# Optimization experiments

Hardware: AMD Instinct MI355X
Metric: run time of the kernel (lower is better)

## Reference

```python
import jax, jax.numpy as jnp
import numpy as np

N_NODES = 100000
N_EDGES = 1600000
IN_CH = 64
HID = 64
OUT_CH = 16
T = 1.0


def _gat_layer(x, edge_index, W, b, t):
    # x: [N, d_in]; W: [d_out, d_in] (torch Linear weight layout); b: [d_out]
    N = x.shape[0]
    loop = jnp.arange(N, dtype=edge_index.dtype)
    src = jnp.concatenate([edge_index[0], loop])  # add self loops
    dst = jnp.concatenate([edge_index[1], loop])
    h = x @ W.T  # [N, d_out]
    x_i = h[dst]  # target node features per edge
    x_j = h[src]  # source node features per edge
    alpha = jnp.sum(x_i * x_j, axis=-1)  # [E']
    alpha = jnp.where(alpha > 0, jnp.asarray(t, h.dtype), jnp.asarray(-t, h.dtype))
    # segment softmax grouped by edge_index[0] (source), faithful to original
    m = jax.ops.segment_max(alpha, src, num_segments=N)
    e = jnp.exp(alpha - m[src])
    s = jax.ops.segment_sum(e, src, num_segments=N)
    w = e / s[src]
    msg = x_j * w[:, None]
    out = jax.ops.segment_sum(msg, dst, num_segments=N)  # scatter-add to target
    return out + b


def setup_inputs() -> dict:
    key = jax.random.key(0)
    k1, k2, k3, k4 = jax.random.split(key, 4)
    x = jax.random.normal(k1, (N_NODES, IN_CH), dtype=jnp.float32)
    edge_index = jax.random.randint(k2, (2, N_EDGES), 0, N_NODES, dtype=jnp.int64)
    # xavier-uniform-ish linear weights, torch layout [out, in]
    lim1 = float(np.sqrt(6.0 / (IN_CH + HID)))
    W1 = jax.random.uniform(k3, (HID, IN_CH), jnp.float32, -lim1, lim1)
    lim2 = float(np.sqrt(6.0 / (HID + OUT_CH)))
    W2 = jax.random.uniform(k4, (OUT_CH, HID), jnp.float32, -lim2, lim2)
    b1 = jnp.zeros((HID,), jnp.float32)
    b2 = jnp.zeros((OUT_CH,), jnp.float32)
    return {"x": x, "edge_index": edge_index, "W1": W1, "b1": b1, "W2": W2, "b2": b2}


def reference(x, edge_index, W1, b1, W2, b2):
    h = _gat_layer(x, edge_index, W1, b1, T)
    h = jax.nn.relu(h)
    h = _gat_layer(h, edge_index, W2, b2, T)
    return jax.nn.log_softmax(h, axis=1)
```

## Files before the change

### kernel.cpp

```cpp
#include <hip/hip_runtime.h>

#define EXPC 0.13533528323661270f
#define REP 8
#define CHUNK 16384

__global__ void zero_i32(int* __restrict__ p, int n) {
  int i = blockIdx.x * blockDim.x + threadIdx.x;
  if (i < n) p[i] = 0;
}

template <bool RELU_IN>
__global__ void __launch_bounds__(256, 1)
gemm64_k(const float* __restrict__ x, const float* __restrict__ W,
         float* __restrict__ h, int N) {
  __shared__ float xs[64][68];
  __shared__ float wt[64][68];
  const int t = threadIdx.x;
  const int r0 = blockIdx.x * 64;
  for (int i = t; i < 4096; i += 256) {
    int c = i >> 6, k = i & 63;
    wt[k][c] = W[i];
  }
  for (int s = t; s < 1024; s += 256) {
    int r = s >> 4, c4 = (s & 15) << 2;
    float4 v = make_float4(0.f, 0.f, 0.f, 0.f);
    if (r0 + r < N) {
      v = *(const float4*)(x + (size_t)(r0 + r) * 64 + c4);
      if (RELU_IN) {
        v.x = fmaxf(v.x, 0.f); v.y = fmaxf(v.y, 0.f);
        v.z = fmaxf(v.z, 0.f); v.w = fmaxf(v.w, 0.f);
      }
    }
    *(float4*)(&xs[r][c4]) = v;
  }
  __syncthreads();
  const int ty = t >> 4, tx = t & 15;
  float acc[4][4] = {};
  for (int kk = 0; kk < 64; kk += 4) {
    float4 a[4], w[4];
#pragma unroll
    for (int i = 0; i < 4; i++) a[i] = *(const float4*)(&xs[4 * ty + i][kk]);
#pragma unroll
    for (int m = 0; m < 4; m++) w[m] = *(const float4*)(&wt[kk + m][4 * tx]);
#pragma unroll
    for (int i = 0; i < 4; i++) {
      acc[i][0] = fmaf(a[i].x, w[0].x, fmaf(a[i].y, w[1].x,
                  fmaf(a[i].z, w[2].x, fmaf(a[i].w, w[3].x, acc[i][0]))));
      acc[i][1] = fmaf(a[i].x, w[0].y, fmaf(a[i].y, w[1].y,
                  fmaf(a[i].z, w[2].y, fmaf(a[i].w, w[3].y, acc[i][1]))));
      acc[i][2] = fmaf(a[i].x, w[0].z, fmaf(a[i].y, w[1].z,
                  fmaf(a[i].z, w[2].z, fmaf(a[i].w, w[3].z, acc[i][2]))));
      acc[i][3] = fmaf(a[i].x, w[0].w, fmaf(a[i].y, w[1].w,
                  fmaf(a[i].z, w[2].w, fmaf(a[i].w, w[3].w, acc[i][3]))));
    }
  }
#pragma unroll
  for (int i = 0; i < 4; i++) {
    int row = r0 + 4 * ty + i;
    if (row < N)
      *(float4*)(h + (size_t)row * 64 + 4 * tx) =
          make_float4(acc[i][0], acc[i][1], acc[i][2], acc[i][3]);
  }
}

template <bool RELU_IN>
__global__ void __launch_bounds__(256, 2)
gemm16_k(const float* __restrict__ x, const float* __restrict__ W,
         float* __restrict__ h, int N) {
  __shared__ float xs[64][68];
  __shared__ float wt[64][20];
  const int t = threadIdx.x;
  const int r0 = blockIdx.x * 64;
  for (int i = t; i < 1024; i += 256) {
    int c = i >> 6, k = i & 63;
    wt[k][c] = W[i];
  }
  for (int s = t; s < 1024; s += 256) {
    int r = s >> 4, c4 = (s & 15) << 2;
    float4 v = make_float4(0.f, 0.f, 0.f, 0.f);
    if (r0 + r < N) {
      v = *(const float4*)(x + (size_t)(r0 + r) * 64 + c4);
      if (RELU_IN) {
        v.x = fmaxf(v.x, 0.f); v.y = fmaxf(v.y, 0.f);
        v.z = fmaxf(v.z, 0.f); v.w = fmaxf(v.w, 0.f);
      }
    }
    *(float4*)(&xs[r][c4]) = v;
  }
  __syncthreads();
  const int r = t >> 2, j = (t & 3) << 2;
  float4 acc = make_float4(0.f, 0.f, 0.f, 0.f);
  for (int k = 0; k < 64; k++) {
    float a = xs[r][k];
    float4 w = *(const float4*)(&wt[k][j]);
    acc.x = fmaf(a, w.x, acc.x);
    acc.y = fmaf(a, w.y, acc.y);
    acc.z = fmaf(a, w.z, acc.z);
    acc.w = fmaf(a, w.w, acc.w);
  }
  int row = r0 + r;
  if (row < N) *(float4*)(h + (size_t)row * 16 + j) = acc;
}

__global__ void passA_k(const int* __restrict__ ei, int* __restrict__ chd,
                        int* __restrict__ chs, int E, int Et) {
  __shared__ int ld[512], ls[512];
  int t = threadIdx.x;
  for (int i = t; i < 512; i += 256) { ld[i] = 0; ls[i] = 0; }
  __syncthreads();
  int base = blockIdx.x * CHUNK;
  int end = base + CHUNK; if (end > Et) end = Et;
  for (int e = base + t; e < end; e += 256) {
    int s, d;
    if (e < E) { s = ei[e]; d = ei[E + e]; } else { s = e - E; d = s; }
    atomicAdd(&ld[d >> 8], 1);
    atomicAdd(&ls[s >> 8], 1);
  }
  __syncthreads();
  for (int i = t; i < 512; i += 256) {
    if (ld[i]) atomicAdd(chd + i, ld[i]);
    if (ls[i]) atomicAdd(chs + i, ls[i]);
  }
}

__global__ void scan2_k(const int* __restrict__ chd, const int* __restrict__ chs,
                        int* __restrict__ cbd, int* __restrict__ cbs,
                        int* __restrict__ cud, int* __restrict__ cus, int NB) {
  __shared__ int l[512];
  int t = threadIdx.x;
  for (int pass = 0; pass < 2; ++pass) {
    const int* src = pass ? chs : chd;
    int* db = pass ? cbs : cbd;
    int* dc = pass ? cus : cud;
    int v = (t < NB) ? src[t] : 0;
    l[t] = v;
    __syncthreads();
    for (int o = 1; o < 512; o <<= 1) {
      int a = (t >= o) ? l[t - o] : 0;
      __syncthreads();
      l[t] += a;
      __syncthreads();
    }
    if (t < NB) { int e = l[t] - v; db[t] = e; dc[t] = e; }
    __syncthreads();
  }
}

__global__ void passB_k(const int* __restrict__ ei, int* __restrict__ cud,
                        int* __restrict__ cus, int* __restrict__ part_dst,
                        unsigned char* __restrict__ part_src, int E, int Et) {
  __shared__ int cntd[512], cnts[512], based[512], bases[512];
  int t = threadIdx.x;
  for (int i = t; i < 512; i += 256) { cntd[i] = 0; cnts[i] = 0; }
  __syncthreads();
  int base = blockIdx.x * CHUNK;
  int end = base + CHUNK; if (end > Et) end = Et;
  for (int e = base + t; e < end; e += 256) {
    int s, d;
    if (e < E) { s = ei[e]; d = ei[E + e]; } else { s = e - E; d = s; }
    atomicAdd(&cntd[d >> 8], 1);
    atomicAdd(&cnts[s >> 8], 1);
  }
  __syncthreads();
  for (int i = t; i < 512; i += 256) {
    based[i] = cntd[i] ? atomicAdd(cud + i, cntd[i]) : 0;
    bases[i] = cnts[i] ? atomicAdd(cus + i, cnts[i]) : 0;
    cntd[i] = 0; cnts[i] = 0;
  }
  __syncthreads();
  for (int e = base + t; e < end; e += 256) {
    int s, d;
    if (e < E) { s = ei[e]; d = ei[E + e]; } else { s = e - E; d = s; }
    int bd = d >> 8, bs = s >> 8;
    int rd = atomicAdd(&cntd[bd], 1);
    int rs = atomicAdd(&cnts[bs], 1);
    part_dst[based[bd] + rd] = s | ((d & 255) << 17);
    part_src[bases[bs] + rs] = (unsigned char)(s & 255);
  }
}

__global__ void passC_k(const int* __restrict__ part_dst, const int* __restrict__ cbd,
                        const int* __restrict__ chd, int* __restrict__ csr_src,
                        int* __restrict__ in_deg, int* __restrict__ off, int N) {
  __shared__ int hist[256], loff[256], rank[256];
  int b = blockIdx.x, t = threadIdx.x;
  int segbase = cbd[b], segcnt = chd[b];
  hist[t] = 0; rank[t] = 0;
  __syncthreads();
  for (int i = t; i < segcnt; i += 256)
    atomicAdd(&hist[part_dst[segbase + i] >> 17], 1);
  __syncthreads();
  int x = hist[t];
  loff[t] = x;
  __syncthreads();
  for (int o = 1; o < 256; o <<= 1) {
    int a = (t >= o) ? loff[t - o] : 0;
    __syncthreads();
    loff[t] += a;
    __syncthreads();
  }
  int excl = loff[t] - x;
  int node = (b << 8) + t;
  if (node < N) { in_deg[node] = x; off[node] = segbase + excl; }
  __syncthreads();
  loff[t] = excl;
  __syncthreads();
  for (int i = t; i < segcnt; i += 256) {
    int rec = part_dst[segbase + i];
    int dl = rec >> 17;
    int r = atomicAdd(&rank[dl], 1);
    csr_src[segbase + loff[dl] + r] = rec & 0x1FFFF;
  }
}

__global__ void passCs_k(const unsigned char* __restrict__ part_src,
                         const int* __restrict__ cbs, const int* __restrict__ chs,
                         int* __restrict__ deg, int N) {
  __shared__ int hist[256];
  int b = blockIdx.x, t = threadIdx.x;
  int segbase = cbs[b], segcnt = chs[b];
  hist[t] = 0;
  __syncthreads();
  for (int i = t; i < segcnt; i += 256)
    atomicAdd(&hist[part_src[segbase + i]], 1);
  __syncthreads();
  int node = (b << 8) + t;
  if (node < N) deg[node] = hist[t];
}

template <int D>
__global__ void alpha_csr_k(const int* __restrict__ csr_src, const int* __restrict__ off,
                            const int* __restrict__ indeg, const float* __restrict__ h,
                            unsigned char* __restrict__ flagb, int* __restrict__ pos_rep,
                            int N) {
  const int G = D / 4;
  int t = blockIdx.x * 256 + threadIdx.x;
  int node = t / G;
  int c = t & (G - 1);
  if (node >= N) return;
  int* pos = pos_rep + (blockIdx.x & (REP - 1)) * N;
  const float4 hd = *(const float4*)(h + (size_t)node * D + c * 4);
  int j = off[node];
  int je = j + indeg[node];
  for (; j + 4 <= je; j += 4) {
    int s0 = csr_src[j], s1 = csr_src[j + 1], s2 = csr_src[j + 2], s3 = csr_src[j + 3];
    float4 a0 = *(const float4*)(h + (size_t)s0 * D + c * 4);
    float4 a1 = *(const float4*)(h + (size_t)s1 * D + c * 4);
    float4 a2 = *(const float4*)(h + (size_t)s2 * D + c * 4);
    float4 a3 = *(const float4*)(h + (size_t)s3 * D + c * 4);
    float p0 = fmaf(a0.x, hd.x, fmaf(a0.y, hd.y, fmaf(a0.z, hd.z, a0.w * hd.w)));
    float p1 = fmaf(a1.x, hd.x, fmaf(a1.y, hd.y, fmaf(a1.z, hd.z, a1.w * hd.w)));
    float p2 = fmaf(a2.x, hd.x, fmaf(a2.y, hd.y, fmaf(a2.z, hd.z, a2.w * hd.w)));
    float p3 = fmaf(a3.x, hd.x, fmaf(a3.y, hd.y, fmaf(a3.z, hd.z, a3.w * hd.w)));
#pragma unroll
    for (int o = G / 2; o > 0; o >>= 1) {
      p0 += __shfl_xor(p0, o);
      p1 += __shfl_xor(p1, o);
      p2 += __shfl_xor(p2, o);
      p3 += __shfl_xor(p3, o);
    }
    if (c == 0) {
      bool z0 = p0 > 0.f, z1 = p1 > 0.f, z2 = p2 > 0.f, z3 = p3 > 0.f;
      flagb[j] = z0; flagb[j + 1] = z1; flagb[j + 2] = z2; flagb[j + 3] = z3;
      if (z0) atomicAdd(pos + s0, 1);
      if (z1) atomicAdd(pos + s1, 1);
      if (z2) atomicAdd(pos + s2, 1);
      if (z3) atomicAdd(pos + s3, 1);
    }
  }
  for (; j < je; ++j) {
    int s = csr_src[j];
    float4 hs = *(const float4*)(h + (size_t)s * D + c * 4);
    float p = fmaf(hs.x, hd.x, fmaf(hs.y, hd.y, fmaf(hs.z, hd.z, hs.w * hd.w)));
#pragma unroll
    for (int o = G / 2; o > 0; o >>= 1) p += __shfl_xor(p, o);
    if (c == 0) {
      bool pz = p > 0.f;
      flagb[j] = (unsigned char)pz;
      if (pz) atomicAdd(pos + s, 1);
    }
  }
}

template <int D>
__global__ void denom_scale_k(const int* __restrict__ pos_rep, const int* __restrict__ deg,
                              float* __restrict__ h, int N) {
  const int G = D / 4;
  int t = blockIdx.x * 256 + threadIdx.x;
  int node = t / G;
  int c = t & (G - 1);
  if (node >= N) return;
  float dinv = 0.f;
  if (c == 0) {
    int p = 0;
#pragma unroll
    for (int r = 0; r < REP; r++) p += pos_rep[r * N + node];
    int dg = deg[node];
    dinv = (p > 0) ? 1.f / ((float)p + (float)(dg - p) * EXPC)
                   : 1.f / (EXPC * (float)dg);
  }
  dinv = __shfl(dinv, 0, G);
  float4* hp = (float4*)(h + (size_t)node * D + c * 4);
  float4 v = *hp;
  v.x *= dinv; v.y *= dinv; v.z *= dinv; v.w *= dinv;
  *hp = v;
}

template <int D, bool FUSE_LSM>
__global__ void gather_csr_k(const int* __restrict__ csr_src, const int* __restrict__ off,
                             const int* __restrict__ indeg,
                             const unsigned char* __restrict__ flagb,
                             const float* __restrict__ h,
                             const float* __restrict__ b, float* __restrict__ outp, int N) {
  const int G = D / 4;
  int t = blockIdx.x * 256 + threadIdx.x;
  int node = t / G;
  int c = t & (G - 1);
  if (node >= N) return;
  float4 acc = *(const float4*)(b + c * 4);
  int j = off[node];
  int je = j + indeg[node];
  for (; j + 4 <= je; j += 4) {
    int s0 = csr_src[j], s1 = csr_src[j + 1], s2 = csr_src[j + 2], s3 = csr_src[j + 3];
    float w0 = flagb[j] ? 1.f : EXPC;
    float w1 = flagb[j + 1] ? 1.f : EXPC;
    float w2 = flagb[j + 2] ? 1.f : EXPC;
    float w3 = flagb[j + 3] ? 1.f : EXPC;
    float4 v0 = *(const float4*)(h + (size_t)s0 * D + c * 4);
    float4 v1 = *(const float4*)(h + (size_t)s1 * D + c * 4);
    float4 v2 = *(const float4*)(h + (size_t)s2 * D + c * 4);
    float4 v3 = *(const float4*)(h + (size_t)s3 * D + c * 4);
    acc.x = fmaf(w0, v0.x, fmaf(w1, v1.x, fmaf(w2, v2.x, fmaf(w3, v3.x, acc.x))));
    acc.y = fmaf(w0, v0.y, fmaf(w1, v1.y, fmaf(w2, v2.y, fmaf(w3, v3.y, acc.y))));
    acc.z = fmaf(w0, v0.z, fmaf(w1, v1.z, fmaf(w2, v2.z, fmaf(w3, v3.z, acc.z))));
    acc.w = fmaf(w0, v0.w, fmaf(w1, v1.w, fmaf(w2, v2.w, fmaf(w3, v3.w, acc.w))));
  }
  for (; j < je; ++j) {
    int s = csr_src[j];
    float w = flagb[j] ? 1.f : EXPC;
    float4 hv = *(const float4*)(h + (size_t)s * D + c * 4);
    acc.x = fmaf(w, hv.x, acc.x);
    acc.y = fmaf(w, hv.y, acc.y);
    acc.z = fmaf(w, hv.z, acc.z);
    acc.w = fmaf(w, hv.w, acc.w);
  }
  if (FUSE_LSM) {
    float m = fmaxf(fmaxf(acc.x, acc.y), fmaxf(acc.z, acc.w));
    m = fmaxf(m, __shfl_xor(m, 1));
    m = fmaxf(m, __shfl_xor(m, 2));
    float s = expf(acc.x - m) + expf(acc.y - m) + expf(acc.z - m) + expf(acc.w - m);
    s += __shfl_xor(s, 1);
    s += __shfl_xor(s, 2);
    float lse = m + logf(s);
    acc.x -= lse; acc.y -= lse; acc.z -= lse; acc.w -= lse;
  }
  *(float4*)(outp + (size_t)node * D + c * 4) = acc;
}

extern "C" void kernel_launch(void* const* d_in, const int* in_sizes, int n_in,
                              void* d_out, int out_size, void* d_ws, size_t ws_size,
                              hipStream_t stream) {
  const float* x = (const float*)d_in[0];
  const int* ei = (const int*)d_in[1];
  const float* W1 = (const float*)d_in[2];
  const float* b1 = (const float*)d_in[3];
  const float* W2 = (const float*)d_in[4];
  const float* b2 = (const float*)d_in[5];
  float* out = (float*)d_out;

  const int N = in_sizes[0] / 64;
  const int E = in_sizes[1] / 2;
  const int Et = E + N;
  const int B = 256;
  const int nbT = (N + 63) / 64;
  const int NB = (N + 255) >> 8;
  const int nbP = (Et + CHUNK - 1) / CHUNK;

  char* ws = (char*)d_ws;
  float* h1 = (float*)ws;    ws += (size_t)N * 64 * 4;
  float* agg1 = (float*)ws;  ws += (size_t)N * 64 * 4;
  int* deg = (int*)ws;       ws += (size_t)N * 4;
  int* in_deg = (int*)ws;    ws += (size_t)N * 4;
  int* off = (int*)ws;       ws += (size_t)N * 4;
  int* chd = (int*)ws;       ws += 512 * 4;
  int* chs = (int*)ws;       ws += 512 * 4;
  int* cbd = (int*)ws;       ws += 512 * 4;
  int* cbs = (int*)ws;       ws += 512 * 4;
  int* cud = (int*)ws;       ws += 512 * 4;
  int* cus = (int*)ws;       ws += 512 * 4;
  int* csr_src = (int*)ws;   ws += (size_t)Et * 4;
  char* P = ws;              ws += (size_t)Et * 4 + (size_t)Et;
  int* part_dst = (int*)P;
  unsigned char* part_src = (unsigned char*)(P + (size_t)Et * 4);
  int* pos_rep = (int*)P;
  unsigned char* flagb = (unsigned char*)(P + (size_t)REP * N * 4);

  hipLaunchKernelGGL(zero_i32, dim3(4), dim3(B), 0, stream, chd, 1024);
  hipLaunchKernelGGL(passA_k, dim3(nbP), dim3(B), 0, stream, ei, chd, chs, E, Et);
  hipLaunchKernelGGL(scan2_k, dim3(1), dim3(512), 0, stream, chd, chs, cbd, cbs, cud, cus, NB);
  hipLaunchKernelGGL(passB_k, dim3(nbP), dim3(B), 0, stream, ei, cud, cus,
                     part_dst, part_src, E, Et);
  hipLaunchKernelGGL(passC_k, dim3(NB), dim3(B), 0, stream, part_dst, cbd, chd,
                     csr_src, in_deg, off, N);
  hipLaunchKernelGGL(passCs_k, dim3(NB), dim3(B), 0, stream, part_src, cbs, chs, deg, N);

  hipLaunchKernelGGL((gemm64_k<false>), dim3(nbT), dim3(B), 0, stream, x, W1, h1, N);
  hipLaunchKernelGGL(zero_i32, dim3((REP * N + B - 1) / B), dim3(B), 0, stream,
                     pos_rep, REP * N);
  hipLaunchKernelGGL((alpha_csr_k<64>), dim3(((size_t)N * 16 + B - 1) / B), dim3(B), 0,
                     stream, csr_src, off, in_deg, h1, flagb, pos_rep, N);
  hipLaunchKernelGGL((denom_scale_k<64>), dim3(((size_t)N * 16 + B - 1) / B), dim3(B), 0,
                     stream, pos_rep, deg, h1, N);
  hipLaunchKernelGGL((gather_csr_k<64, false>), dim3(((size_t)N * 16 + B - 1) / B), dim3(B),
                     0, stream, csr_src, off, in_deg, flagb, h1, b1, agg1, N);

  float* h2 = h1;
  hipLaunchKernelGGL((gemm16_k<true>), dim3(nbT), dim3(B), 0, stream, agg1, W2, h2, N);
  hipLaunchKernelGGL(zero_i32, dim3((REP * N + B - 1) / B), dim3(B), 0, stream,
                     pos_rep, REP * N);
  hipLaunchKernelGGL((alpha_csr_k<16>), dim3(((size_t)N * 4 + B - 1) / B), dim3(B), 0,
                     stream, csr_src, off, in_deg, h2, flagb, pos_rep, N);
  hipLaunchKernelGGL((denom_scale_k<16>), dim3(((size_t)N * 4 + B - 1) / B), dim3(B), 0,
                     stream, pos_rep, deg, h2, N);
  hipLaunchKernelGGL((gather_csr_k<16, true>), dim3(((size_t)N * 4 + B - 1) / B), dim3(B),
                     0, stream, csr_src, off, in_deg, flagb, h2, b2, out, N);
}
```

Before: 486.5 us.

## Fuse layer-2 GEMM and ReLU into layer-1 gather, unroll edge loops by 8

The layer-1 gather now applies ReLU and multiplies by W2 in registers: the 16 lanes of a node share the aggregated row through shuffles and write h2 directly. This removes the agg1 buffer write, the separate gemm16 kernel and its re-read of 64-wide rows. The alpha and gather edge loops are unrolled from 4 to 8 so more gathers are in flight at once, at the cost of more registers per thread. __launch_bounds__(256,1) is added to the alpha and gather kernels.

```diff
diff --git a/kernel.cpp b/kernel.cpp
--- a/kernel.cpp
+++ b/kernel.cpp
@@ -61,45 +61,6 @@
       *(float4*)(h + (size_t)row * 64 + 4 * tx) =
           make_float4(acc[i][0], acc[i][1], acc[i][2], acc[i][3]);
   }
-}
-
-template <bool RELU_IN>
-__global__ void __launch_bounds__(256, 2)
-gemm16_k(const float* __restrict__ x, const float* __restrict__ W,
-         float* __restrict__ h, int N) {
-  __shared__ float xs[64][68];
-  __shared__ float wt[64][20];
-  const int t = threadIdx.x;
-  const int r0 = blockIdx.x * 64;
-  for (int i = t; i < 1024; i += 256) {
-    int c = i >> 6, k = i & 63;
-    wt[k][c] = W[i];
-  }
-  for (int s = t; s < 1024; s += 256) {
-    int r = s >> 4, c4 = (s & 15) << 2;
-    float4 v = make_float4(0.f, 0.f, 0.f, 0.f);
-    if (r0 + r < N) {
-      v = *(const float4*)(x + (size_t)(r0 + r) * 64 + c4);
-      if (RELU_IN) {
-        v.x = fmaxf(v.x, 0.f); v.y = fmaxf(v.y, 0.f);
-        v.z = fmaxf(v.z, 0.f); v.w = fmaxf(v.w, 0.f);
-      }
-    }
-    *(float4*)(&xs[r][c4]) = v;
-  }
-  __syncthreads();
-  const int r = t >> 2, j = (t & 3) << 2;
-  float4 acc = make_float4(0.f, 0.f, 0.f, 0.f);
-  for (int k = 0; k < 64; k++) {
-    float a = xs[r][k];
-    float4 w = *(const float4*)(&wt[k][j]);
-    acc.x = fmaf(a, w.x, acc.x);
-    acc.y = fmaf(a, w.y, acc.y);
-    acc.z = fmaf(a, w.z, acc.z);
-    acc.w = fmaf(a, w.w, acc.w);
-  }
-  int row = r0 + r;
-  if (row < N) *(float4*)(h + (size_t)row * 16 + j) = acc;
 }
 
 __global__ void passA_k(const int* __restrict__ ei, int* __restrict__ chd,
@@ -229,10 +190,10 @@
 }
 
 template <int D>
-__global__ void alpha_csr_k(const int* __restrict__ csr_src, const int* __restrict__ off,
-                            const int* __restrict__ indeg, const float* __restrict__ h,
-                            unsigned char* __restrict__ flagb, int* __restrict__ pos_rep,
-                            int N) {
+__global__ void __launch_bounds__(256, 1)
+alpha_csr_k(const int* __restrict__ csr_src, const int* __restrict__ off,
+            const int* __restrict__ indeg, const float* __restrict__ h,
+            unsigned char* __restrict__ flagb, int* __restrict__ pos_rep, int N) {
   const int G = D / 4;
   int t = blockIdx.x * 256 + threadIdx.x;
   int node = t / G;
@@ -242,30 +203,29 @@
   const float4 hd = *(const float4*)(h + (size_t)node * D + c * 4);
   int j = off[node];
   int je = j + indeg[node];
-  for (; j + 4 <= je; j += 4) {
-    int s0 = csr_src[j], s1 = csr_src[j + 1], s2 = csr_src[j + 2], s3 = csr_src[j + 3];
-    float4 a0 = *(const float4*)(h + (size_t)s0 * D + c * 4);
-    float4 a1 = *(const float4*)(h + (size_t)s1 * D + c * 4);
-    float4 a2 = *(const float4*)(h + (size_t)s2 * D + c * 4);
-    float4 a3 = *(const float4*)(h + (size_t)s3 * D + c * 4);
-    float p0 = fmaf(a0.x, hd.x, fmaf(a0.y, hd.y, fmaf(a0.z, hd.z, a0.w * hd.w)));
-    float p1 = fmaf(a1.x, hd.x, fmaf(a1.y, hd.y, fmaf(a1.z, hd.z, a1.w * hd.w)));
-    float p2 = fmaf(a2.x, hd.x, fmaf(a2.y, hd.y, fmaf(a2.z, hd.z, a2.w * hd.w)));
-    float p3 = fmaf(a3.x, hd.x, fmaf(a3.y, hd.y, fmaf(a3.z, hd.z, a3.w * hd.w)));
+  for (; j + 8 <= je; j += 8) {
+    int s[8];
+    float4 a[8];
+#pragma unroll
+    for (int u = 0; u < 8; u++) s[u] = csr_src[j + u];
+#pragma unroll
+    for (int u = 0; u < 8; u++) a[u] = *(const float4*)(h + (size_t)s[u] * D + c * 4);
+    float p[8];
+#pragma unroll
+    for (int u = 0; u < 8; u++)
+      p[u] = fmaf(a[u].x, hd.x, fmaf(a[u].y, hd.y, fmaf(a[u].z, hd.z, a[u].w * hd.w)));
 #pragma unroll
     for (int o = G / 2; o > 0; o >>= 1) {
-      p0 += __shfl_xor(p0, o);
-      p1 += __shfl_xor(p1, o);
-      p2 += __shfl_xor(p2, o);
-      p3 += __shfl_xor(p3, o);
+#pragma unroll
+      for (int u = 0; u < 8; u++) p[u] += __shfl_xor(p[u], o);
     }
     if (c == 0) {
-      bool z0 = p0 > 0.f, z1 = p1 > 0.f, z2 = p2 > 0.f, z3 = p3 > 0.f;
-      flagb[j] = z0; flagb[j + 1] = z1; flagb[j + 2] = z2; flagb[j + 3] = z3;
-      if (z0) atomicAdd(pos + s0, 1);
-      if (z1) atomicAdd(pos + s1, 1);
-      if (z2) atomicAdd(pos + s2, 1);
-      if (z3) atomicAdd(pos + s3, 1);
+#pragma unroll
+      for (int u = 0; u < 8; u++) {
+        bool z = p[u] > 0.f;
+        flagb[j + u] = (unsigned char)z;
+        if (z) atomicAdd(pos + s[u], 1);
+      }
     }
   }
   for (; j < je; ++j) {
@@ -306,55 +266,114 @@
   *hp = v;
 }
 
-template <int D, bool FUSE_LSM>
-__global__ void gather_csr_k(const int* __restrict__ csr_src, const int* __restrict__ off,
-                             const int* __restrict__ indeg,
-                             const unsigned char* __restrict__ flagb,
-                             const float* __restrict__ h,
-                             const float* __restrict__ b, float* __restrict__ outp, int N) {
-  const int G = D / 4;
-  int t = blockIdx.x * 256 + threadIdx.x;
-  int node = t / G;
-  int c = t & (G - 1);
+__global__ void __launch_bounds__(256, 1)
+gather1_g16_k(const int* __restrict__ csr_src, const int* __restrict__ off,
+              const int* __restrict__ indeg, const unsigned char* __restrict__ flagb,
+              const float* __restrict__ h, const float* __restrict__ b1,
+              const float* __restrict__ W2, float* __restrict__ h2, int N) {
+  __shared__ float wt2[16][68];
+  const int t = threadIdx.x;
+  for (int i = t; i < 1024; i += 256) wt2[i >> 6][i & 63] = W2[i];
+  __syncthreads();
+  int g = blockIdx.x * 256 + t;
+  int node = g >> 4;
+  int c = g & 15;
   if (node >= N) return;
-  float4 acc = *(const float4*)(b + c * 4);
+  float4 acc = *(const float4*)(b1 + c * 4);
   int j = off[node];
   int je = j + indeg[node];
-  for (; j + 4 <= je; j += 4) {
-    int s0 = csr_src[j], s1 = csr_src[j + 1], s2 = csr_src[j + 2], s3 = csr_src[j + 3];
-    float w0 = flagb[j] ? 1.f : EXPC;
-    float w1 = flagb[j + 1] ? 1.f : EXPC;
-    float w2 = flagb[j + 2] ? 1.f : EXPC;
-    float w3 = flagb[j + 3] ? 1.f : EXPC;
-    float4 v0 = *(const float4*)(h + (size_t)s0 * D + c * 4);
-    float4 v1 = *(const float4*)(h + (size_t)s1 * D + c * 4);
-    float4 v2 = *(const float4*)(h + (size_t)s2 * D + c * 4);
-    float4 v3 = *(const float4*)(h + (size_t)s3 * D + c * 4);
-    acc.x = fmaf(w0, v0.x, fmaf(w1, v1.x, fmaf(w2, v2.x, fmaf(w3, v3.x, acc.x))));
-    acc.y = fmaf(w0, v0.y, fmaf(w1, v1.y, fmaf(w2, v2.y, fmaf(w3, v3.y, acc.y))));
-    acc.z = fmaf(w0, v0.z, fmaf(w1, v1.z, fmaf(w2, v2.z, fmaf(w3, v3.z, acc.z))));
-    acc.w = fmaf(w0, v0.w, fmaf(w1, v1.w, fmaf(w2, v2.w, fmaf(w3, v3.w, acc.w))));
+  for (; j + 8 <= je; j += 8) {
+    int s[8];
+    float w[8];
+    float4 v[8];
+#pragma unroll
+    for (int u = 0; u < 8; u++) s[u] = csr_src[j + u];
+#pragma unroll
+    for (int u = 0; u < 8; u++) w[u] = flagb[j + u] ? 1.f : EXPC;
+#pragma unroll
+    for (int u = 0; u < 8; u++) v[u] = *(const float4*)(h + (size_t)s[u] * 64 + c * 4);
+#pragma unroll
+    for (int u = 0; u < 8; u++) {
+      acc.x = fmaf(w[u], v[u].x, acc.x);
+      acc.y = fmaf(w[u], v[u].y, acc.y);
+      acc.z = fmaf(w[u], v[u].z, acc.z);
+      acc.w = fmaf(w[u], v[u].w, acc.w);
+    }
   }
   for (; j < je; ++j) {
     int s = csr_src[j];
     float w = flagb[j] ? 1.f : EXPC;
-    float4 hv = *(const float4*)(h + (size_t)s * D + c * 4);
+    float4 hv = *(const float4*)(h + (size_t)s * 64 + c * 4);
     acc.x = fmaf(w, hv.x, acc.x);
     acc.y = fmaf(w, hv.y, acc.y);
     acc.z = fmaf(w, hv.z, acc.z);
     acc.w = fmaf(w, hv.w, acc.w);
   }
-  if (FUSE_LSM) {
-    float m = fmaxf(fmaxf(acc.x, acc.y), fmaxf(acc.z, acc.w));
-    m = fmaxf(m, __shfl_xor(m, 1));
-    m = fmaxf(m, __shfl_xor(m, 2));
-    float s = expf(acc.x - m) + expf(acc.y - m) + expf(acc.z - m) + expf(acc.w - m);
-    s += __shfl_xor(s, 1);
-    s += __shfl_xor(s, 2);
-    float lse = m + logf(s);
-    acc.x -= lse; acc.y -= lse; acc.z -= lse; acc.w -= lse;
-  }
-  *(float4*)(outp + (size_t)node * D + c * 4) = acc;
+  acc.x = fmaxf(acc.x, 0.f); acc.y = fmaxf(acc.y, 0.f);
+  acc.z = fmaxf(acc.z, 0.f); acc.w = fmaxf(acc.w, 0.f);
+  int lanebase = (threadIdx.x & 63) & 48;
+  float o = 0.f;
+#pragma unroll
+  for (int s16 = 0; s16 < 16; s16++) {
+    int src = lanebase + s16;
+    float cx = __shfl(acc.x, src);
+    float cy = __shfl(acc.y, src);
+    float cz = __shfl(acc.z, src);
+    float cw = __shfl(acc.w, src);
+    float4 wv = *(const float4*)(&wt2[c][4 * s16]);
+    o = fmaf(cx, wv.x, fmaf(cy, wv.y, fmaf(cz, wv.z, fmaf(cw, wv.w, o))));
+  }
+  h2[(size_t)node * 16 + c] = o;
+}
+
+__global__ void __launch_bounds__(256, 1)
+gather2_k(const int* __restrict__ csr_src, const int* __restrict__ off,
+          const int* __restrict__ indeg, const unsigned char* __restrict__ flagb,
+          const float* __restrict__ h, const float* __restrict__ b2,
+          float* __restrict__ outp, int N) {
+  int t = blockIdx.x * 256 + threadIdx.x;
+  int node = t >> 2;
+  int c = t & 3;
+  if (node >= N) return;
+  float4 acc = *(const float4*)(b2 + c * 4);
+  int j = off[node];
+  int je = j + indeg[node];
+  for (; j + 8 <= je; j += 8) {
+    int s[8];
+    float w[8];
+    float4 v[8];
+#pragma unroll
+    for (int u = 0; u < 8; u++) s[u] = csr_src[j + u];
+#pragma unroll
+    for (int u = 0; u < 8; u++) w[u] = flagb[j + u] ? 1.f : EXPC;
+#pragma unroll
+    for (int u = 0; u < 8; u++) v[u] = *(const float4*)(h + (size_t)s[u] * 16 + c * 4);
+#pragma unroll
+    for (int u = 0; u < 8; u++) {
+      acc.x = fmaf(w[u], v[u].x, acc.x);
+      acc.y = fmaf(w[u], v[u].y, acc.y);
+      acc.z = fmaf(w[u], v[u].z, acc.z);
+      acc.w = fmaf(w[u], v[u].w, acc.w);
+    }
+  }
+  for (; j < je; ++j) {
+    int s = csr_src[j];
+    float w = flagb[j] ? 1.f : EXPC;
+    float4 hv = *(const float4*)(h + (size_t)s * 16 + c * 4);
+    acc.x = fmaf(w, hv.x, acc.x);
+    acc.y = fmaf(w, hv.y, acc.y);
+    acc.z = fmaf(w, hv.z, acc.z);
+    acc.w = fmaf(w, hv.w, acc.w);
+  }
+  float m = fmaxf(fmaxf(acc.x, acc.y), fmaxf(acc.z, acc.w));
+  m = fmaxf(m, __shfl_xor(m, 1));
+  m = fmaxf(m, __shfl_xor(m, 2));
+  float s = expf(acc.x - m) + expf(acc.y - m) + expf(acc.z - m) + expf(acc.w - m);
+  s += __shfl_xor(s, 1);
+  s += __shfl_xor(s, 2);
+  float lse = m + logf(s);
+  acc.x -= lse; acc.y -= lse; acc.z -= lse; acc.w -= lse;
+  *(float4*)(outp + (size_t)node * 16 + c * 4) = acc;
 }
 
 extern "C" void kernel_launch(void* const* d_in, const int* in_sizes, int n_in,
@@ -378,7 +397,7 @@
 
   char* ws = (char*)d_ws;
   float* h1 = (float*)ws;    ws += (size_t)N * 64 * 4;
-  float* agg1 = (float*)ws;  ws += (size_t)N * 64 * 4;
+  float* h2 = (float*)ws;    ws += (size_t)N * 16 * 4;
   int* deg = (int*)ws;       ws += (size_t)N * 4;
   int* in_deg = (int*)ws;    ws += (size_t)N * 4;
   int* off = (int*)ws;       ws += (size_t)N * 4;
@@ -411,17 +430,15 @@
                      stream, csr_src, off, in_deg, h1, flagb, pos_rep, N);
   hipLaunchKernelGGL((denom_scale_k<64>), dim3(((size_t)N * 16 + B - 1) / B), dim3(B), 0,
                      stream, pos_rep, deg, h1, N);
-  hipLaunchKernelGGL((gather_csr_k<64, false>), dim3(((size_t)N * 16 + B - 1) / B), dim3(B),
-                     0, stream, csr_src, off, in_deg, flagb, h1, b1, agg1, N);
-
-  float* h2 = h1;
-  hipLaunchKernelGGL((gemm16_k<true>), dim3(nbT), dim3(B), 0, stream, agg1, W2, h2, N);
+  hipLaunchKernelGGL(gather1_g16_k, dim3(((size_t)N * 16 + B - 1) / B), dim3(B), 0,
+                     stream, csr_src, off, in_deg, flagb, h1, b1, W2, h2, N);
+
   hipLaunchKernelGGL(zero_i32, dim3((REP * N + B - 1) / B), dim3(B), 0, stream,
                      pos_rep, REP * N);
   hipLaunchKernelGGL((alpha_csr_k<16>), dim3(((size_t)N * 4 + B - 1) / B), dim3(B), 0,
                      stream, csr_src, off, in_deg, h2, flagb, pos_rep, N);
   hipLaunchKernelGGL((denom_scale_k<16>), dim3(((size_t)N * 4 + B - 1) / B), dim3(B), 0,
                      stream, pos_rep, deg, h2, N);
-  hipLaunchKernelGGL((gather_csr_k<16, true>), dim3(((size_t)N * 4 + B - 1) / B), dim3(B),
-                     0, stream, csr_src, off, in_deg, flagb, h2, b2, out, N);
-}
+  hipLaunchKernelGGL(gather2_k, dim3(((size_t)N * 4 + B - 1) / B), dim3(B), 0,
+                     stream, csr_src, off, in_deg, flagb, h2, b2, out, N);
+}
```

After: 490.0 us. About the same (+0.7%).
